# Kernel tuning notes

Measured on AMD Instinct MI355X. Metric: run time of the kernel, lower is better.

## Reference

```python
import jax, jax.numpy as jnp
import numpy as np

D = 512
LD = 2
NTR = 16384
NT = 8192
NCLS = 16

def setup_inputs() -> dict:
    key = jax.random.key(0)
    k1, k2, k3, k4 = jax.random.split(key, 4)
    xtr = jax.random.normal(k1, (NTR, D), dtype=jnp.float32)
    ytr = jax.random.normal(k2, (NTR, NCLS), dtype=jnp.float32)
    xt = jax.random.normal(k3, (NT, D), dtype=jnp.float32)
    # original: A ~ U[0,1)/sqrt(d), shape (ld, d), used as x @ A with A stored (d, ld) here
    A = jax.random.uniform(k4, (D, LD), dtype=jnp.float32) / jnp.sqrt(jnp.float32(D))
    return {"xtr": xtr, "ytr": ytr, "xt": xt, "A": A}

def reference(xtr, ytr, xt, A):
    # low-rank projections: [Nt, ld], [Ntr, ld]
    q = xt @ A
    k = xtr @ A
    # similarity logits [Nt, Ntr], softmax over train points, weighted label agg
    E = jax.nn.softmax(q @ k.T, axis=1)
    return E @ ytr
```

## Files before the change

### kernel.cpp

```cpp
#include <hip/hip_runtime.h>
#include <hip/hip_bf16.h>
#include <math.h>

#define DIM   512
#define NTR   16384
#define NT    8192
#define NCLS  16
#define NROWS (NTR + NT)

#define JS     16
#define JC     (NTR / JS)
#define STEPS  (JC / 32)
#define NSTEPS (NTR / 32)

#define PROJ_BLOCKS (NROWS / 16)
#define PREP_BLOCKS ((NSTEPS * 64) / 256)

#define WS_KQ_F    (NROWS * 2)
#define WS_YFH_S   (NSTEPS * 64 * 8)
#define WS_NPART_F (JS * NT * NCLS)
#define WS_DPART_F (JS * NT)

typedef __attribute__((ext_vector_type(8))) short short8;
typedef __attribute__((ext_vector_type(4))) float f32x4;
typedef __attribute__((ext_vector_type(4))) unsigned int uint4v;

static __device__ __forceinline__ short f2bf(float f) {
    unsigned u = __float_as_uint(f);
    return (short)((u + 0x7FFFu + ((u >> 16) & 1u)) >> 16);
}
static __device__ __forceinline__ unsigned pkbf(float a, float b) {
    unsigned ua = __float_as_uint(a) + 0x8000u;
    unsigned ub = __float_as_uint(b) + 0x8000u;
    return __builtin_amdgcn_perm(ub, ua, 0x07060302);
}

__global__ __launch_bounds__(256) void prep_kernel(
    const float* __restrict__ xtr, const float* __restrict__ xt,
    const float* __restrict__ A, const float* __restrict__ ytr,
    float* __restrict__ kq, short* __restrict__ yfh)
{
    const int b = blockIdx.x;
    if (b < PROJ_BLOCKS) {
        const int wave = threadIdx.x >> 6;
        const int lane = threadIdx.x & 63;
        const int row0 = b * 16 + wave * 4;

        const float* xp[4];
#pragma unroll
        for (int r = 0; r < 4; ++r) {
            const int row = row0 + r;
            xp[r] = (row < NTR) ? (xtr + (size_t)row * DIM)
                                : (xt + (size_t)(row - NTR) * DIM);
        }
        float a0[4] = {0.f, 0.f, 0.f, 0.f}, a1[4] = {0.f, 0.f, 0.f, 0.f};
#pragma unroll
        for (int t = 0; t < 2; ++t) {
            const int d = lane * 4 + t * 256;
            float4 A0 = *(const float4*)(A + 2 * d);
            float4 A1 = *(const float4*)(A + 2 * d + 4);
#pragma unroll
            for (int r = 0; r < 4; ++r) {
                float4 u = *(const float4*)(xp[r] + d);
                a0[r] += u.x * A0.x + u.y * A0.z + u.z * A1.x + u.w * A1.z;
                a1[r] += u.x * A0.y + u.y * A0.w + u.z * A1.y + u.w * A1.w;
            }
        }
#pragma unroll
        for (int off = 32; off >= 1; off >>= 1) {
#pragma unroll
            for (int r = 0; r < 4; ++r) {
                a0[r] += __shfl_xor(a0[r], off, 64);
                a1[r] += __shfl_xor(a1[r], off, 64);
            }
        }
        if (lane == 0) {
            *(float4*)(kq + row0 * 2)     = make_float4(a0[0], a1[0], a0[1], a1[1]);
            *(float4*)(kq + row0 * 2 + 4) = make_float4(a0[2], a1[2], a0[3], a1[3]);
        }
    } else {
        const int idx = (b - PROJ_BLOCKS) * 256 + threadIdx.x;
        const int l   = idx & 63;
        const int s   = idx >> 6;
        const int cls = l & 15;
        const int jb  = s * 32 + (l >> 4) * 8;
        short8 hi;
#pragma unroll
        for (int t = 0; t < 8; ++t)
            hi[t] = f2bf(ytr[(size_t)(jb + t) * NCLS + cls]);
        ((short8*)yfh)[idx] = hi;
    }
}

__global__ __launch_bounds__(512) void simmain_kernel(
    const float* __restrict__ kq, const short* __restrict__ yfh,
    float* __restrict__ npart, float* __restrict__ dpart)
{
    __shared__ float  ks[JC * 2];
    __shared__ short8 ys[STEPS * 64];

    const int tid  = threadIdx.x;
    const int wave = tid >> 6;
    const int lane = tid & 63;
    const int j0   = blockIdx.y * JC;

    const int i0   = (blockIdx.x * 8 + wave) * 16;
    const int m    = lane & 15;
    const int quad = lane >> 4;

    const float2 qv = *(const float2*)(kq + 2 * (NTR + i0 + m));
    const float q0 = qv.x * 1.4426950408889634f;
    const float q1 = qv.y * 1.4426950408889634f;

    {
        const float4* ksrc = (const float4*)(kq + 2 * j0);
        ((float4*)ks)[tid] = ksrc[tid];
        const float4* ysrc = (const float4*)(yfh + (size_t)blockIdx.y * (STEPS * 64) * 8);
        float4* ydst = (float4*)ys;
#pragma unroll
        for (int p = 0; p < 4; ++p)
            ydst[tid + 512 * p] = ysrc[tid + 512 * p];
    }
    __syncthreads();

    f32x4 acc  = {0.f, 0.f, 0.f, 0.f};
    f32x4 acc2 = {0.f, 0.f, 0.f, 0.f};
    short8 ones;
#pragma unroll
    for (int t = 0; t < 8; ++t) ones[t] = (short)0x3F80;

    const short8* __restrict__ yls = ys + lane;
    const float4* __restrict__ kx  = ((const float4*)ks) + quad * 4;

#pragma unroll 4
    for (int s = 0; s < STEPS; ++s) {
        const short8 yh = yls[s * 64];
        const float4* kp = kx + s * 16;
        const float4 ka = kp[0], kb = kp[1], kc = kp[2], kd = kp[3];

        const float e0 = __builtin_amdgcn_exp2f(fmaf(q1, ka.y, q0 * ka.x));
        const float e1 = __builtin_amdgcn_exp2f(fmaf(q1, ka.w, q0 * ka.z));
        const float e2 = __builtin_amdgcn_exp2f(fmaf(q1, kb.y, q0 * kb.x));
        const float e3 = __builtin_amdgcn_exp2f(fmaf(q1, kb.w, q0 * kb.z));
        const float e4 = __builtin_amdgcn_exp2f(fmaf(q1, kc.y, q0 * kc.x));
        const float e5 = __builtin_amdgcn_exp2f(fmaf(q1, kc.w, q0 * kc.z));
        const float e6 = __builtin_amdgcn_exp2f(fmaf(q1, kd.y, q0 * kd.x));
        const float e7 = __builtin_amdgcn_exp2f(fmaf(q1, kd.w, q0 * kd.z));

        uint4v ep;
        ep[0] = pkbf(e0, e1); ep[1] = pkbf(e2, e3);
        ep[2] = pkbf(e4, e5); ep[3] = pkbf(e6, e7);
        const short8 eb = __builtin_bit_cast(short8, ep);

        acc  = __builtin_amdgcn_mfma_f32_16x16x32_bf16(yh,   eb, acc,  0, 0, 0);
        acc2 = __builtin_amdgcn_mfma_f32_16x16x32_bf16(ones, eb, acc2, 0, 0, 0);
    }

    float* np = npart + ((size_t)blockIdx.y * NT + (i0 + m)) * NCLS + quad * 4;
    *(float4*)np = make_float4(acc[0], acc[1], acc[2], acc[3]);
    if (quad == 0)
        dpart[blockIdx.y * NT + i0 + m] = acc2[0];
}

__global__ __launch_bounds__(256) void finalize_kernel(
    const float* __restrict__ npart, const float* __restrict__ dpart,
    float* __restrict__ out)
{
    const int idx = blockIdx.x * 256 + threadIdx.x;
    const int i = idx >> 4;
    float n = 0.f, d = 0.f;
#pragma unroll
    for (int s = 0; s < JS; ++s) {
        n += npart[(size_t)s * (NT * NCLS) + idx];
        d += dpart[s * NT + i];
    }
    out[idx] = n / d;
}

extern "C" void kernel_launch(void* const* d_in, const int* in_sizes, int n_in,
                              void* d_out, int out_size, void* d_ws, size_t ws_size,
                              hipStream_t stream)
{
    const float* xtr = (const float*)d_in[0];
    const float* ytr = (const float*)d_in[1];
    const float* xt  = (const float*)d_in[2];
    const float* A   = (const float*)d_in[3];
    float* out = (float*)d_out;

    float* kq    = (float*)d_ws;
    short* yfh   = (short*)(kq + WS_KQ_F);
    float* npart = (float*)(yfh + WS_YFH_S);
    float* dpart = npart + WS_NPART_F;

    prep_kernel<<<PROJ_BLOCKS + PREP_BLOCKS, 256, 0, stream>>>(
        xtr, xt, A, ytr, kq, yfh);
    simmain_kernel<<<dim3(NT / 128, JS), 512, 0, stream>>>(
        kq, yfh, npart, dpart);
    finalize_kernel<<<(NT * NCLS) / 256, 256, 0, stream>>>(npart, dpart, out);
}
```

Baseline: 111.8 us.

## Split k into planar layout, read keys from global, use packed FMA and bf16 cvt

The projection output changes from interleaved (k0,k1) pairs to two planar arrays. The main kernel now reads keys straight from global memory (through cache) instead of staging them in LDS. Logits are computed with v_pk_mul/v_pk_fma on pairs, and bf16 packing uses the hardware v_cvt_pk_bf16_f32 instruction. This is meant to cut VALU instruction count per step and LDS traffic, at the cost of global/L1 loads inside the hot loop and a smaller unroll.

Result: slower. 123.8 us (+10.7%).

```diff
diff --git a/kernel.cpp b/kernel.cpp
--- a/kernel.cpp
+++ b/kernel.cpp
@@ -23,16 +23,30 @@
 
 typedef __attribute__((ext_vector_type(8))) short short8;
 typedef __attribute__((ext_vector_type(4))) float f32x4;
+typedef __attribute__((ext_vector_type(2))) float f32x2;
 typedef __attribute__((ext_vector_type(4))) unsigned int uint4v;
 
 static __device__ __forceinline__ short f2bf(float f) {
     unsigned u = __float_as_uint(f);
     return (short)((u + 0x7FFFu + ((u >> 16) & 1u)) >> 16);
 }
-static __device__ __forceinline__ unsigned pkbf(float a, float b) {
-    unsigned ua = __float_as_uint(a) + 0x8000u;
-    unsigned ub = __float_as_uint(b) + 0x8000u;
-    return __builtin_amdgcn_perm(ub, ua, 0x07060302);
+static __device__ __forceinline__ f32x2 mk2(float x, float y) {
+    f32x2 r; r[0] = x; r[1] = y; return r;
+}
+static __device__ __forceinline__ f32x2 pk_fma(f32x2 a, f32x2 b, f32x2 c) {
+    f32x2 d;
+    asm("v_pk_fma_f32 %0, %1, %2, %3" : "=v"(d) : "v"(a), "v"(b), "v"(c));
+    return d;
+}
+static __device__ __forceinline__ f32x2 pk_mul(f32x2 a, f32x2 b) {
+    f32x2 d;
+    asm("v_pk_mul_f32 %0, %1, %2" : "=v"(d) : "v"(a), "v"(b));
+    return d;
+}
+static __device__ __forceinline__ unsigned cvtpk(float a, float b) {
+    unsigned d;
+    asm("v_cvt_pk_bf16_f32 %0, %1, %2" : "=v"(d) : "v"(a), "v"(b));
+    return d;
 }
 
 __global__ __launch_bounds__(256) void prep_kernel(
@@ -75,8 +89,8 @@
             }
         }
         if (lane == 0) {
-            *(float4*)(kq + row0 * 2)     = make_float4(a0[0], a1[0], a0[1], a1[1]);
-            *(float4*)(kq + row0 * 2 + 4) = make_float4(a0[2], a1[2], a0[3], a1[3]);
+            *(float4*)(kq + row0)         = make_float4(a0[0], a0[1], a0[2], a0[3]);
+            *(float4*)(kq + NROWS + row0) = make_float4(a1[0], a1[1], a1[2], a1[3]);
         }
     } else {
         const int idx = (b - PROJ_BLOCKS) * 256 + threadIdx.x;
@@ -96,7 +110,6 @@
     const float* __restrict__ kq, const short* __restrict__ yfh,
     float* __restrict__ npart, float* __restrict__ dpart)
 {
-    __shared__ float  ks[JC * 2];
     __shared__ short8 ys[STEPS * 64];
 
     const int tid  = threadIdx.x;
@@ -108,13 +121,12 @@
     const int m    = lane & 15;
     const int quad = lane >> 4;
 
-    const float2 qv = *(const float2*)(kq + 2 * (NTR + i0 + m));
-    const float q0 = qv.x * 1.4426950408889634f;
-    const float q1 = qv.y * 1.4426950408889634f;
+    const float q0 = kq[NTR + i0 + m]         * 1.4426950408889634f;
+    const float q1 = kq[NROWS + NTR + i0 + m] * 1.4426950408889634f;
+    const f32x2 q00 = mk2(q0, q0);
+    const f32x2 q11 = mk2(q1, q1);
 
     {
-        const float4* ksrc = (const float4*)(kq + 2 * j0);
-        ((float4*)ks)[tid] = ksrc[tid];
         const float4* ysrc = (const float4*)(yfh + (size_t)blockIdx.y * (STEPS * 64) * 8);
         float4* ydst = (float4*)ys;
 #pragma unroll
@@ -130,26 +142,34 @@
     for (int t = 0; t < 8; ++t) ones[t] = (short)0x3F80;
 
     const short8* __restrict__ yls = ys + lane;
-    const float4* __restrict__ kx  = ((const float4*)ks) + quad * 4;
-
-#pragma unroll 4
+    const float* __restrict__ kq0 = kq + j0 + quad * 8;
+    const float* __restrict__ kq1 = kq + NROWS + j0 + quad * 8;
+
+#pragma unroll 2
     for (int s = 0; s < STEPS; ++s) {
         const short8 yh = yls[s * 64];
-        const float4* kp = kx + s * 16;
-        const float4 ka = kp[0], kb = kp[1], kc = kp[2], kd = kp[3];
-
-        const float e0 = __builtin_amdgcn_exp2f(fmaf(q1, ka.y, q0 * ka.x));
-        const float e1 = __builtin_amdgcn_exp2f(fmaf(q1, ka.w, q0 * ka.z));
-        const float e2 = __builtin_amdgcn_exp2f(fmaf(q1, kb.y, q0 * kb.x));
-        const float e3 = __builtin_amdgcn_exp2f(fmaf(q1, kb.w, q0 * kb.z));
-        const float e4 = __builtin_amdgcn_exp2f(fmaf(q1, kc.y, q0 * kc.x));
-        const float e5 = __builtin_amdgcn_exp2f(fmaf(q1, kc.w, q0 * kc.z));
-        const float e6 = __builtin_amdgcn_exp2f(fmaf(q1, kd.y, q0 * kd.x));
-        const float e7 = __builtin_amdgcn_exp2f(fmaf(q1, kd.w, q0 * kd.z));
+        const float4 a0 = *(const float4*)(kq0 + s * 32);
+        const float4 b0 = *(const float4*)(kq0 + s * 32 + 4);
+        const float4 a1 = *(const float4*)(kq1 + s * 32);
+        const float4 b1 = *(const float4*)(kq1 + s * 32 + 4);
+
+        const f32x2 l0 = pk_fma(q11, mk2(a1.x, a1.y), pk_mul(q00, mk2(a0.x, a0.y)));
+        const f32x2 l1 = pk_fma(q11, mk2(a1.z, a1.w), pk_mul(q00, mk2(a0.z, a0.w)));
+        const f32x2 l2 = pk_fma(q11, mk2(b1.x, b1.y), pk_mul(q00, mk2(b0.x, b0.y)));
+        const f32x2 l3 = pk_fma(q11, mk2(b1.z, b1.w), pk_mul(q00, mk2(b0.z, b0.w)));
+
+        const float e0 = __builtin_amdgcn_exp2f(l0[0]);
+        const float e1 = __builtin_amdgcn_exp2f(l0[1]);
+        const float e2 = __builtin_amdgcn_exp2f(l1[0]);
+        const float e3 = __builtin_amdgcn_exp2f(l1[1]);
+        const float e4 = __builtin_amdgcn_exp2f(l2[0]);
+        const float e5 = __builtin_amdgcn_exp2f(l2[1]);
+        const float e6 = __builtin_amdgcn_exp2f(l3[0]);
+        const float e7 = __builtin_amdgcn_exp2f(l3[1]);
 
         uint4v ep;
-        ep[0] = pkbf(e0, e1); ep[1] = pkbf(e2, e3);
-        ep[2] = pkbf(e4, e5); ep[3] = pkbf(e6, e7);
+        ep[0] = cvtpk(e0, e1); ep[1] = cvtpk(e2, e3);
+        ep[2] = cvtpk(e4, e5); ep[3] = cvtpk(e6, e7);
         const short8 eb = __builtin_bit_cast(short8, ep);
 
         acc  = __builtin_amdgcn_mfma_f32_16x16x32_bf16(yh,   eb, acc,  0, 0, 0);
```
